# Optimization experiments

Measured on AMD Instinct MI355X. Metric: run time of the kernel, lower is better.

The kernel has to match this reference:

```python
import jax, jax.numpy as jnp
import numpy as np

B, S, H, NH = 4, 2048, 512, 8  # batch, seq, hidden, heads
D = H // NH                    # head dim = 64


def setup_inputs() -> dict:
    key = jax.random.key(0)
    ks = jax.random.split(key, 12)
    wscale = 1.0 / np.sqrt(H)
    mk = lambda k, sh: jax.random.normal(k, sh, jnp.float32)
    return {
        "q": mk(ks[0], (B, S, H)),
        "k": mk(ks[1], (B, S, H)),
        "v": mk(ks[2], (B, S, H)),
        "k_b": mk(ks[3], (B, S, H)),
        "mask": jax.random.randint(ks[4], (B, S), 0, 2).astype(jnp.int32),
        "Wq": mk(ks[5], (H, H)) * wscale, "bq": jnp.zeros((H,), jnp.float32),
        "Wk": mk(ks[6], (H, H)) * wscale, "bk": jnp.zeros((H,), jnp.float32),
        "Wv": mk(ks[7], (H, H)) * wscale, "bv": jnp.zeros((H,), jnp.float32),
        "Wkb": mk(ks[8], (H, H)) * wscale, "bkb": jnp.zeros((H,), jnp.float32),
        "Wo": mk(ks[9], (H, H)) * wscale, "bo": jnp.zeros((H,), jnp.float32),
    }


def _attn(q, k, v, k_b, mask, Wq, bq, Wk, bk, Wv, bv, Wkb, bkb, Wo, bo):
    b, s, h = q.shape
    proj = lambda x, W, bias: (x @ W + bias).reshape(b, s, NH, D).transpose(0, 2, 1, 3)
    qh = proj(q, Wq, bq)      # [b, nh, s, d]
    kh = proj(k, Wk, bk)
    vh = proj(v, Wv, bv)
    kbh = proj(k_b, Wkb, bkb)
    # q@k^T + q@k_b^T == q@(k+k_b)^T, scaled by sqrt(d)
    corr = jnp.einsum('bhqd,bhkd->bhqk', qh, kh + kbh) / jnp.sqrt(jnp.float32(D))
    # torch mask repeat pattern depends only on key index -> broadcast over q and heads
    corr = jnp.where(mask[:, None, None, :] == 0, jnp.float32(-1e9), corr)
    prob = jax.nn.softmax(corr, axis=-1)  # dropout inactive (eval mode)
    hid = jnp.einsum('bhqk,bhkd->bhqd', prob, vh)
    hid = hid.transpose(0, 2, 1, 3).reshape(b, s, h)
    return hid @ Wo + bo


def reference(q, k, v, k_b, mask, Wq, bq, Wk, bk, Wv, bv, Wkb, bkb, Wo, bo):
    return _attn(q, k, v, k_b, mask, Wq, bq, Wk, bk, Wv, bv, Wkb, bkb, Wo, bo)
```

## Files before the change

### kernel.cpp

```cpp
#include <hip/hip_runtime.h>
#include <hip/hip_bf16.h>
#include <math.h>

#define B_  4
#define S_  2048
#define H_  512
#define NH_ 8
#define D_  64

typedef __attribute__((ext_vector_type(8))) short bf16x8;
typedef __attribute__((ext_vector_type(4))) float f32x4;
typedef __attribute__((ext_vector_type(16))) float f32x16;
#define MFMA16(a, b, c) __builtin_amdgcn_mfma_f32_16x16x32_bf16(a, b, c, 0, 0, 0)
#define MFMA32(a, b, c) __builtin_amdgcn_mfma_f32_32x32x16_bf16(a, b, c, 0, 0, 0)

__device__ __forceinline__ unsigned short f2bf(float f) {
    union { float f; unsigned int i; } x; x.f = f;
    unsigned int i = x.i;
    i += 0x7fffu + ((i >> 16) & 1u);
    return (unsigned short)(i >> 16);
}
__device__ __forceinline__ unsigned int pk2(float lo, float hi) {
    union { __hip_bfloat162 h; unsigned int u; } c;
    c.h = __float22bfloat162_rn(make_float2(lo, hi));
    return c.u;
}
__device__ __forceinline__ void gl_lds16(const void* g, void* l) {
    __builtin_amdgcn_global_load_lds(
        (const __attribute__((address_space(1))) unsigned int*)g,
        (__attribute__((address_space(3))) unsigned int*)l, 16, 0, 0);
}

__global__ __launch_bounds__(256) void prep_w(
    const float* __restrict__ W0, const float* __restrict__ W1,
    const float* __restrict__ W2, const float* __restrict__ W3,
    unsigned short* __restrict__ Wt)
{
    const float* Ws[4] = {W0, W1, W2, W3};
    const float* W = Ws[blockIdx.z];
    unsigned short* Y = Wt + (size_t)blockIdx.z * H_ * H_;
    __shared__ float Tl[64][68];
    const int t = threadIdx.x;
    const int k0 = blockIdx.y * 64, n0 = blockIdx.x * 64;
    #pragma unroll
    for (int i = 0; i < 4; ++i) {
        const int e = (t + 256 * i) * 4;
        const int r = e >> 6, c = e & 63;
        const float4 a = *(const float4*)(W + (size_t)(k0 + r) * H_ + n0 + c);
        Tl[c + 0][r] = a.x; Tl[c + 1][r] = a.y;
        Tl[c + 2][r] = a.z; Tl[c + 3][r] = a.w;
    }
    __syncthreads();
    #pragma unroll
    for (int i = 0; i < 4; ++i) {
        const int e = (t + 256 * i) * 4;
        const int n = e >> 6, c = e & 63;
        uint2 p;
        p.x = pk2(Tl[n][c + 0], Tl[n][c + 1]);
        p.y = pk2(Tl[n][c + 2], Tl[n][c + 3]);
        *(uint2*)(Y + (size_t)(n0 + n) * H_ + k0 + c) = p;
    }
}

__global__ __launch_bounds__(256, 3) void proj_all(
    const float* __restrict__ q,  const float* __restrict__ k,
    const float* __restrict__ v,  const float* __restrict__ k_b,
    const unsigned short* __restrict__ Wt,
    const float* __restrict__ bq, const float* __restrict__ bk,
    const float* __restrict__ bkb,const float* __restrict__ bv,
    unsigned short* __restrict__ Qf, unsigned short* __restrict__ Kf,
    unsigned short* __restrict__ Vf)
{
    __shared__ __align__(16) unsigned short LB[17408];
    unsigned short* As = LB;
    unsigned short* Bs = LB + 8192;

    const int z = blockIdx.z;
    const float *X, *bias, *X2 = nullptr, *bias2 = nullptr;
    const unsigned short *Wa, *Wb = nullptr;
    unsigned short* Y;
    bool VT = false;
    const size_t WSZ = (size_t)H_ * H_;
    if (z == 0)      { X = q; Wa = Wt;           bias = bq; Y = Qf; }
    else if (z == 1) { X = k; Wa = Wt + WSZ;     bias = bk;
                       X2 = k_b; Wb = Wt + 2 * WSZ; bias2 = bkb; Y = Kf; }
    else             { X = v; Wa = Wt + 3 * WSZ; bias = bv; Y = Vf; VT = true; }

    const int t = threadIdx.x;
    const int w = t >> 6, lane = t & 63;
    const int quad = lane >> 4, l15 = lane & 15;
    const int wr = w >> 1, wc = w & 1;
    const int m0 = blockIdx.x * 128, n0 = blockIdx.y * 128;

    const f32x4 zero = {0.f, 0.f, 0.f, 0.f};
    f32x4 acc[4][4];
    #pragma unroll
    for (int i = 0; i < 4; ++i)
        #pragma unroll
        for (int j = 0; j < 4; ++j) acc[i][j] = zero;

    const int npass = (X2 != nullptr) ? 2 : 1;
    for (int pass = 0; pass < npass; ++pass) {
        const float* Xp = pass ? X2 : X;
        const unsigned short* Wp = pass ? Wb : Wa;
        for (int kb0 = 0; kb0 < H_; kb0 += 64) {
            __syncthreads();
            #pragma unroll
            for (int i = 0; i < 4; ++i) {
                const int c = w * 4 + i;
                const int u = c * 64 + lane;
                const int row = u >> 3;
                const int sc  = ((u & 7) ^ (row & 7)) << 3;
                gl_lds16(Wp + (size_t)(n0 + row) * H_ + kb0 + sc, Bs + c * 512);
            }
            float4 av[8];
            #pragma unroll
            for (int i = 0; i < 8; ++i) {
                const int e = (t + 256 * i) * 4;
                av[i] = *(const float4*)(Xp + (size_t)(m0 + (e >> 6)) * H_ + kb0 + (e & 63));
            }
            #pragma unroll
            for (int i = 0; i < 8; ++i) {
                const int e = (t + 256 * i) * 4;
                const int row = e >> 6, kc = e & 63;
                uint2 p; p.x = pk2(av[i].x, av[i].y); p.y = pk2(av[i].z, av[i].w);
                *(uint2*)&As[row * 64 + ((((kc >> 3) ^ (row & 7)) << 3) | (kc & 7))] = p;
            }
            __syncthreads();
            #pragma unroll
            for (int ks = 0; ks < 2; ++ks) {
                bf16x8 af[4], bfr[4];
                #pragma unroll
                for (int i = 0; i < 4; ++i) {
                    const int row = wr * 64 + i * 16 + l15;
                    af[i] = *(const bf16x8*)&As[row * 64 +
                                (((ks * 4 + quad) ^ (row & 7)) << 3)];
                }
                #pragma unroll
                for (int j = 0; j < 4; ++j) {
                    const int nrw = wc * 64 + j * 16 + l15;
                    bfr[j] = *(const bf16x8*)&Bs[nrw * 64 +
                                (((ks * 4 + quad) ^ (nrw & 7)) << 3)];
                }
                #pragma unroll
                for (int i = 0; i < 4; ++i)
                    #pragma unroll
                    for (int j = 0; j < 4; ++j)
                        acc[i][j] = MFMA16(af[i], bfr[j], acc[i][j]);
            }
        }
    }

    const int bb = m0 >> 11, s0 = m0 & (S_ - 1);
    if (!VT) {
        #pragma unroll
        for (int i = 0; i < 4; ++i)
            #pragma unroll
            for (int r = 0; r < 4; ++r) {
                const int s = s0 + wr * 64 + i * 16 + quad * 4 + r;
                #pragma unroll
                for (int j = 0; j < 4; ++j) {
                    const int nn = n0 + wc * 64 + j * 16 + l15;
                    const int h = nn >> 6, d = nn & 63;
                    float val = acc[i][j][r] + bias[nn];
                    if (bias2) val += bias2[nn];
                    Y[(((size_t)bb * NH_ + h) * S_ + s) * D_ + d] = f2bf(val);
                }
            }
    } else {
        __syncthreads();
        #pragma unroll
        for (int i = 0; i < 4; ++i)
            #pragma unroll
            for (int r = 0; r < 4; ++r) {
                const int ml = wr * 64 + i * 16 + quad * 4 + r;
                #pragma unroll
                for (int j = 0; j < 4; ++j) {
                    const int nl = wc * 64 + j * 16 + l15;
                    LB[nl * 136 + ml] = f2bf(acc[i][j][r] + bias[n0 + nl]);
                }
            }
        __syncthreads();
        const int nr = t >> 1, half = t & 1;
        const int nn = n0 + nr, h = nn >> 6, d = nn & 63;
        const size_t vbase = (((size_t)bb * NH_ + h) * D_ + d) * S_ + s0 + half * 64;
        #pragma unroll
        for (int i = 0; i < 16; ++i)
            *(ushort4*)(Y + vbase + i * 4) =
                *(const ushort4*)&LB[nr * 136 + half * 64 + i * 4];
    }
}

__global__ __launch_bounds__(256, 4) void attn_mfma(
    unsigned short* QHd,
    const unsigned short* __restrict__ Kh, const unsigned short* __restrict__ Vt,
    const int* __restrict__ mask)
{
    const int b = blockIdx.z, h = blockIdx.y;
    const int q0 = blockIdx.x * 64;
    const int t = threadIdx.x;
    const int w = t >> 6, lane = t & 63;
    const int hi = lane >> 5, l31 = lane & 31;
    const int qg = w & 1, kh = w >> 1;

    __shared__ __align__(16) unsigned short KsL[2 * 4096];
    __shared__ __align__(16) unsigned short VsL[2 * 4096];
    __shared__ float mskf[S_];

    const size_t head = ((size_t)b * NH_ + h) * S_;
    unsigned short* Qbase = QHd + head * D_;
    const unsigned short* Kbase = Kh + head * D_;
    const unsigned short* Vbase = Vt + head * D_;

    for (int i = t; i < S_; i += 256)
        mskf[i] = (mask[b * S_ + i] == 0) ? -1e9f : 0.f;

    bf16x8 qf[4];
    #pragma unroll
    for (int ks = 0; ks < 4; ++ks)
        qf[ks] = *(const bf16x8*)(
            Qbase + (size_t)(q0 + qg * 32 + l31) * D_ + ks * 16 + hi * 8);

    f32x16 O0, O1;
    #pragma unroll
    for (int i = 0; i < 16; ++i) { O0[i] = 0.f; O1[i] = 0.f; }
    float lsum = 0.f;
    const float SC2 = 0.125f * 1.44269504089f;

    #define STAGE(kt_) do {                                                        \
        const int bf_ = (kt_) & 1, k0_ = (kt_) * 64;                               \
        _Pragma("unroll")                                                          \
        for (int i_ = 0; i_ < 2; ++i_) {                                           \
            const int c_ = w * 2 + i_;                                             \
            const int u_ = c_ * 64 + lane;                                         \
            const int row_ = u_ >> 3;                                              \
            const int sc_ = ((u_ & 7) ^ (row_ & 7)) << 3;                          \
            gl_lds16(Kbase + (size_t)(k0_ + row_) * D_ + sc_,                      \
                     KsL + bf_ * 4096 + c_ * 512);                                 \
            gl_lds16(Vbase + (size_t)row_ * S_ + k0_ + sc_,                        \
                     VsL + bf_ * 4096 + c_ * 512);                                 \
        }                                                                          \
    } while (0)

    STAGE(0);
    __syncthreads();

    for (int kt = 0; kt < S_ / 64; ++kt) {
        const int bf = kt & 1;
        const int k0 = kt * 64;
        if (kt + 1 < S_ / 64) STAGE(kt + 1);

        f32x16 acc;
        #pragma unroll
        for (int i = 0; i < 16; ++i) acc[i] = 0.f;
        const int krow = kh * 32 + l31;
        const unsigned short* Kb = KsL + bf * 4096 + krow * 64;
        const int rwk = krow & 7;
        __builtin_amdgcn_s_setprio(1);
        #pragma unroll
        for (int ks = 0; ks < 4; ++ks) {
            const bf16x8 kf = *(const bf16x8*)&Kb[(((ks * 2 + hi) ^ rwk) << 3)];
            acc = MFMA32(kf, qf[ks], acc);
        }
        __builtin_amdgcn_s_setprio(0);
        float p[16];
        #pragma unroll
        for (int bq = 0; bq < 4; ++bq) {
            const float4 ms4 = *(const float4*)&mskf[k0 + kh * 32 + bq * 8 + hi * 4];
            p[4 * bq + 0] = __builtin_amdgcn_exp2f(fmaf(acc[4 * bq + 0], SC2, ms4.x));
            p[4 * bq + 1] = __builtin_amdgcn_exp2f(fmaf(acc[4 * bq + 1], SC2, ms4.y));
            p[4 * bq + 2] = __builtin_amdgcn_exp2f(fmaf(acc[4 * bq + 2], SC2, ms4.z));
            p[4 * bq + 3] = __builtin_amdgcn_exp2f(fmaf(acc[4 * bq + 3], SC2, ms4.w));
        }
        lsum += ((p[0] + p[1]) + (p[2] + p[3])) + ((p[4] + p[5]) + (p[6] + p[7]))
              + ((p[8] + p[9]) + (p[10] + p[11])) + ((p[12] + p[13]) + (p[14] + p[15]));
        unsigned pkv[8];
        #pragma unroll
        for (int bq = 0; bq < 4; ++bq) {
            pkv[2 * bq + 0] = pk2(p[4 * bq + 0], p[4 * bq + 1]);
            pkv[2 * bq + 1] = pk2(p[4 * bq + 2], p[4 * bq + 3]);
        }
        bf16x8 pfrag[2];
        #pragma unroll
        for (int ksl = 0; ksl < 2; ++ksl) {
            unsigned m0 = pkv[4 * ksl + 0], m2 = pkv[4 * ksl + 2];
            asm volatile("v_permlane32_swap_b32 %0, %1" : "+v"(m0), "+v"(m2));
            unsigned m1 = pkv[4 * ksl + 1], m3 = pkv[4 * ksl + 3];
            asm volatile("v_permlane32_swap_b32 %0, %1" : "+v"(m1), "+v"(m3));
            union { unsigned u[4]; bf16x8 v; } pu;
            pu.u[0] = m0; pu.u[1] = m1; pu.u[2] = m2; pu.u[3] = m3;
            pfrag[ksl] = pu.v;
        }
        __builtin_amdgcn_s_setprio(1);
        #pragma unroll
        for (int dblk = 0; dblk < 2; ++dblk) {
            const int vrow = dblk * 32 + l31;
            const unsigned short* Vb = VsL + bf * 4096 + vrow * 64;
            const int rwv = vrow & 7;
            #pragma unroll
            for (int ksl = 0; ksl < 2; ++ksl) {
                const bf16x8 vf =
                    *(const bf16x8*)&Vb[(((kh * 4 + ksl * 2 + hi) ^ rwv) << 3)];
                if (dblk == 0) O0 = MFMA32(vf, pfrag[ksl], O0);
                else           O1 = MFMA32(vf, pfrag[ksl], O1);
            }
        }
        __builtin_amdgcn_s_setprio(0);
        __syncthreads();
    }
    #undef STAGE

    lsum += __shfl_xor(lsum, 32, 64);

    if (kh == 1) {
        float* R = qg ? (float*)VsL : (float*)KsL;
        #pragma unroll
        for (int i = 0; i < 16; ++i) R[lane * 33 + i]      = O0[i];
        #pragma unroll
        for (int i = 0; i < 16; ++i) R[lane * 33 + 16 + i] = O1[i];
        if (hi == 0) R[2112 + l31] = lsum;
    }
    __syncthreads();
    if (kh == 0) {
        const float* R = qg ? (const float*)VsL : (const float*)KsL;
        #pragma unroll
        for (int i = 0; i < 16; ++i) O0[i] += R[lane * 33 + i];
        #pragma unroll
        for (int i = 0; i < 16; ++i) O1[i] += R[lane * 33 + 16 + i];
        lsum += R[2112 + l31];
        const float inv = 1.f / lsum;

        unsigned short* Orow = Qbase + (size_t)(q0 + qg * 32 + l31) * D_;
        #pragma unroll
        for (int dblk = 0; dblk < 2; ++dblk) {
            #pragma unroll
            for (int bq = 0; bq < 4; ++bq) {
                const float v0 = (dblk ? O1[4 * bq + 0] : O0[4 * bq + 0]) * inv;
                const float v1 = (dblk ? O1[4 * bq + 1] : O0[4 * bq + 1]) * inv;
                const float v2 = (dblk ? O1[4 * bq + 2] : O0[4 * bq + 2]) * inv;
                const float v3 = (dblk ? O1[4 * bq + 3] : O0[4 * bq + 3]) * inv;
                uint2 st; st.x = pk2(v0, v1); st.y = pk2(v2, v3);
                *(uint2*)&Orow[dblk * 32 + bq * 8 + hi * 4] = st;
            }
        }
    }
}

__global__ __launch_bounds__(256) void out_mfma(
    const unsigned short* __restrict__ Hd, const unsigned short* __restrict__ Wot,
    const float* __restrict__ bias, float* __restrict__ Out)
{
    __shared__ __align__(16) unsigned short As[8192];
    __shared__ __align__(16) unsigned short Bs[4096];
    const int t = threadIdx.x;
    const int w = t >> 6, lane = t & 63;
    const int quad = lane >> 4, l15 = lane & 15;
    const int wr = w >> 1, wc = w & 1;
    const int m0 = blockIdx.x * 128, n0 = blockIdx.y * 64;
    const int bb = m0 >> 11, s0 = m0 & (S_ - 1);

    const f32x4 zero = {0.f, 0.f, 0.f, 0.f};
    f32x4 acc[4][2];
    #pragma unroll
    for (int i = 0; i < 4; ++i)
        #pragma unroll
        for (int j = 0; j < 2; ++j) acc[i][j] = zero;

    for (int kb0 = 0; kb0 < H_; kb0 += 64) {
        const int hk = kb0 >> 6;
        const unsigned short* Ab = Hd + (((size_t)bb * NH_ + hk) * S_ + s0) * D_;
        __syncthreads();
        #pragma unroll
        for (int i = 0; i < 4; ++i) {
            const int c = w * 4 + i, u = c * 64 + lane, row = u >> 3;
            const int sc = ((u & 7) ^ (row & 7)) << 3;
            gl_lds16(Ab + (size_t)row * D_ + sc, As + c * 512);
        }
        #pragma unroll
        for (int i = 0; i < 2; ++i) {
            const int c = w * 2 + i, u = c * 64 + lane, row = u >> 3;
            const int sc = ((u & 7) ^ (row & 7)) << 3;
            gl_lds16(Wot + (size_t)(n0 + row) * H_ + kb0 + sc, Bs + c * 512);
        }
        __syncthreads();
        #pragma unroll
        for (int ks = 0; ks < 2; ++ks) {
            bf16x8 af[4], bfr[2];
            #pragma unroll
            for (int i = 0; i < 4; ++i) {
                const int row = wr * 64 + i * 16 + l15;
                af[i] = *(const bf16x8*)&As[row * 64 +
                            (((ks * 4 + quad) ^ (row & 7)) << 3)];
            }
            #pragma unroll
            for (int j = 0; j < 2; ++j) {
                const int nrw = wc * 32 + j * 16 + l15;
                bfr[j] = *(const bf16x8*)&Bs[nrw * 64 +
                            (((ks * 4 + quad) ^ (nrw & 7)) << 3)];
            }
            #pragma unroll
            for (int i = 0; i < 4; ++i)
                #pragma unroll
                for (int j = 0; j < 2; ++j)
                    acc[i][j] = MFMA16(af[i], bfr[j], acc[i][j]);
        }
    }
    #pragma unroll
    for (int i = 0; i < 4; ++i)
        #pragma unroll
        for (int r = 0; r < 4; ++r) {
            const int m = m0 + wr * 64 + i * 16 + quad * 4 + r;
            #pragma unroll
            for (int j = 0; j < 2; ++j) {
                const int n = n0 + wc * 32 + j * 16 + l15;
                Out[(size_t)m * H_ + n] = acc[i][j][r] + bias[n];
            }
        }
}

__global__ void fill_kernel(float* __restrict__ out, float val, int n) {
    const int i = blockIdx.x * 256 + threadIdx.x;
    if (i < n) out[i] = val;
}

extern "C" void kernel_launch(void* const* d_in, const int* in_sizes, int n_in,
                              void* d_out, int out_size, void* d_ws, size_t ws_size,
                              hipStream_t stream) {
    const float* q   = (const float*)d_in[0];
    const float* k   = (const float*)d_in[1];
    const float* v   = (const float*)d_in[2];
    const float* k_b = (const float*)d_in[3];
    const int*   msk = (const int*)d_in[4];
    const float* Wq  = (const float*)d_in[5];
    const float* bq  = (const float*)d_in[6];
    const float* Wk  = (const float*)d_in[7];
    const float* bk  = (const float*)d_in[8];
    const float* Wv  = (const float*)d_in[9];
    const float* bv  = (const float*)d_in[10];
    const float* Wkb = (const float*)d_in[11];
    const float* bkb = (const float*)d_in[12];
    const float* Wo  = (const float*)d_in[13];
    const float* bo  = (const float*)d_in[14];
    float* out = (float*)d_out;

    const size_t PER  = (size_t)B_ * NH_ * S_ * D_;
    const size_t NEED = 3 * PER * sizeof(unsigned short);
    if (ws_size < NEED) {
        fill_kernel<<<(out_size + 255) / 256, 256, 0, stream>>>(
            out, (float)((ws_size >> 20) + 2), out_size);
        return;
    }
    unsigned short* wsh = (unsigned short*)d_ws;
    unsigned short* Qf  = wsh;
    unsigned short* Kf  = wsh + PER;
    unsigned short* Vf  = wsh + 2 * PER;

    unsigned short* Wt = (unsigned short*)d_out;

    dim3 gw(8, 8, 4);
    prep_w<<<gw, 256, 0, stream>>>(Wq, Wk, Wkb, Wv, Wt);

    dim3 gp((B_ * S_) / 128, H_ / 128, 3);
    proj_all<<<gp, 256, 0, stream>>>(q, k, v, k_b, Wt, bq, bk, bkb, bv, Qf, Kf, Vf);

    dim3 ga(S_ / 64, NH_, B_);
    attn_mfma<<<ga, 256, 0, stream>>>(Qf, Kf, Vf, msk);

    dim3 gw1(8, 8, 1);
    prep_w<<<gw1, 256, 0, stream>>>(Wo, Wo, Wo, Wo, Kf);

    dim3 go((B_ * S_) / 128, H_ / 64, 1);
    out_mfma<<<go, 256, 0, stream>>>(Qf, Kf, bo, out);
}
```

Baseline: 232.1 us.

## Compute softmax row sums via MFMA and double-buffer output projection loads

The attention kernel drops the scalar per-lane accumulation of exponentials and computes the softmax denominator with an extra MFMA against a ones matrix, which also removes the cross-lane shuffle reduction. The output projection GEMM moves from a single LDS buffer to double buffering, so the next head's tiles are loaded while the current tile is multiplied, with one barrier per step. This trades VALU adds for two extra MFMAs per key tile and a third accumulator (more registers). The GEMM now uses twice the LDS, which may reduce occupancy.

```diff
diff --git a/kernel.cpp b/kernel.cpp
--- a/kernel.cpp
+++ b/kernel.cpp
@@ -221,10 +221,13 @@
         qf[ks] = *(const bf16x8*)(
             Qbase + (size_t)(q0 + qg * 32 + l31) * D_ + ks * 16 + hi * 8);
 
-    f32x16 O0, O1;
-    #pragma unroll
-    for (int i = 0; i < 16; ++i) { O0[i] = 0.f; O1[i] = 0.f; }
-    float lsum = 0.f;
+    bf16x8 onesA;
+    #pragma unroll
+    for (int i = 0; i < 8; ++i) onesA[i] = (short)0x3F80;
+
+    f32x16 O0, O1, O2;
+    #pragma unroll
+    for (int i = 0; i < 16; ++i) { O0[i] = 0.f; O1[i] = 0.f; O2[i] = 0.f; }
     const float SC2 = 0.125f * 1.44269504089f;
 
     #define STAGE(kt_) do {                                                        \
@@ -272,8 +275,6 @@
             p[4 * bq + 2] = __builtin_amdgcn_exp2f(fmaf(acc[4 * bq + 2], SC2, ms4.z));
             p[4 * bq + 3] = __builtin_amdgcn_exp2f(fmaf(acc[4 * bq + 3], SC2, ms4.w));
         }
-        lsum += ((p[0] + p[1]) + (p[2] + p[3])) + ((p[4] + p[5]) + (p[6] + p[7]))
-              + ((p[8] + p[9]) + (p[10] + p[11])) + ((p[12] + p[13]) + (p[14] + p[15]));
         unsigned pkv[8];
         #pragma unroll
         for (int bq = 0; bq < 4; ++bq) {
@@ -305,12 +306,14 @@
                 else           O1 = MFMA32(vf, pfrag[ksl], O1);
             }
         }
+        O2 = MFMA32(onesA, pfrag[0], O2);
+        O2 = MFMA32(onesA, pfrag[1], O2);
         __builtin_amdgcn_s_setprio(0);
         __syncthreads();
     }
     #undef STAGE
 
-    lsum += __shfl_xor(lsum, 32, 64);
+    float lsum = O2[0];
 
     if (kh == 1) {
         float* R = qg ? (float*)VsL : (float*)KsL;
@@ -350,8 +353,8 @@
     const unsigned short* __restrict__ Hd, const unsigned short* __restrict__ Wot,
     const float* __restrict__ bias, float* __restrict__ Out)
 {
-    __shared__ __align__(16) unsigned short As[8192];
-    __shared__ __align__(16) unsigned short Bs[4096];
+    __shared__ __align__(16) unsigned short As2[2][8192];
+    __shared__ __align__(16) unsigned short Bs2[2][4096];
     const int t = threadIdx.x;
     const int w = t >> 6, lane = t & 63;
     const int quad = lane >> 4, l15 = lane & 15;
@@ -366,36 +369,44 @@
         #pragma unroll
         for (int j = 0; j < 2; ++j) acc[i][j] = zero;
 
-    for (int kb0 = 0; kb0 < H_; kb0 += 64) {
-        const int hk = kb0 >> 6;
-        const unsigned short* Ab = Hd + (((size_t)bb * NH_ + hk) * S_ + s0) * D_;
-        __syncthreads();
-        #pragma unroll
-        for (int i = 0; i < 4; ++i) {
-            const int c = w * 4 + i, u = c * 64 + lane, row = u >> 3;
-            const int sc = ((u & 7) ^ (row & 7)) << 3;
-            gl_lds16(Ab + (size_t)row * D_ + sc, As + c * 512);
-        }
-        #pragma unroll
-        for (int i = 0; i < 2; ++i) {
-            const int c = w * 2 + i, u = c * 64 + lane, row = u >> 3;
-            const int sc = ((u & 7) ^ (row & 7)) << 3;
-            gl_lds16(Wot + (size_t)(n0 + row) * H_ + kb0 + sc, Bs + c * 512);
-        }
-        __syncthreads();
+    #define OSTAGE(s_, bfx_) do {                                              \
+        const int hk_ = (s_);                                                  \
+        const unsigned short* Ab_ = Hd + (((size_t)bb * NH_ + hk_) * S_ + s0)  \
+                                    * D_;                                      \
+        _Pragma("unroll")                                                      \
+        for (int i_ = 0; i_ < 4; ++i_) {                                       \
+            const int c_ = w * 4 + i_, u_ = c_ * 64 + lane, row_ = u_ >> 3;    \
+            const int sc_ = ((u_ & 7) ^ (row_ & 7)) << 3;                      \
+            gl_lds16(Ab_ + (size_t)row_ * D_ + sc_, As2[bfx_] + c_ * 512);     \
+        }                                                                      \
+        _Pragma("unroll")                                                      \
+        for (int i_ = 0; i_ < 2; ++i_) {                                       \
+            const int c_ = w * 2 + i_, u_ = c_ * 64 + lane, row_ = u_ >> 3;    \
+            const int sc_ = ((u_ & 7) ^ (row_ & 7)) << 3;                      \
+            gl_lds16(Wot + (size_t)(n0 + row_) * H_ + hk_ * 64 + sc_,          \
+                     Bs2[bfx_] + c_ * 512);                                    \
+        }                                                                      \
+    } while (0)
+
+    OSTAGE(0, 0);
+    __syncthreads();
+
+    for (int s = 0; s < 8; ++s) {
+        const int cur = s & 1;
+        if (s + 1 < 8) OSTAGE(s + 1, cur ^ 1);
         #pragma unroll
         for (int ks = 0; ks < 2; ++ks) {
             bf16x8 af[4], bfr[2];
             #pragma unroll
             for (int i = 0; i < 4; ++i) {
                 const int row = wr * 64 + i * 16 + l15;
-                af[i] = *(const bf16x8*)&As[row * 64 +
+                af[i] = *(const bf16x8*)&As2[cur][row * 64 +
                             (((ks * 4 + quad) ^ (row & 7)) << 3)];
             }
             #pragma unroll
             for (int j = 0; j < 2; ++j) {
                 const int nrw = wc * 32 + j * 16 + l15;
-                bfr[j] = *(const bf16x8*)&Bs[nrw * 64 +
+                bfr[j] = *(const bf16x8*)&Bs2[cur][nrw * 64 +
                             (((ks * 4 + quad) ^ (nrw & 7)) << 3)];
             }
             #pragma unroll
@@ -404,7 +415,10 @@
                 for (int j = 0; j < 2; ++j)
                     acc[i][j] = MFMA16(af[i], bfr[j], acc[i][j]);
         }
-    }
+        __syncthreads();
+    }
+    #undef OSTAGE
+
     #pragma unroll
     for (int i = 0; i < 4; ++i)
         #pragma unroll
```

Result: no change. 232.1 us (+0.0%).
